# Kernel tuning notes

Measured on AMD Instinct MI355X. Metric: run time of the kernel, lower is better.

## Reference

```python
import jax, jax.numpy as jnp
import numpy as np

N_NODES = 50000
N_EDGES = 300000
D_IN = 256
D_OUT = 256


def setup_inputs() -> dict:
    key = jax.random.key(0)
    k1, k2, k3, k4 = jax.random.split(key, 4)
    x = jax.random.normal(k1, (N_NODES, D_IN), dtype=jnp.float32)
    edge_index = jax.random.randint(k2, (2, N_EDGES), 0, N_NODES, dtype=jnp.int64)
    edge_weight = jax.random.uniform(k3, (N_EDGES,), dtype=jnp.float32)
    # nn.Linear(D_IN, D_OUT, bias=False): weight shape [out, in]
    W = jax.random.normal(k4, (D_OUT, D_IN), dtype=jnp.float32) * (1.0 / np.sqrt(D_IN))
    return {"x": x, "edge_index": edge_index, "edge_weight": edge_weight, "W": W}


def reference(x, edge_index, edge_weight, W):
    # x = self.linear(x)  -> [N, D_OUT]
    x_proj = jnp.einsum("nd,od->no", x, W)
    # torch.sparse.mm(A_hat, x_proj): out[dst] += A[dst, src] * x_proj[src]
    dst = edge_index[0]
    src = edge_index[1]
    msgs = edge_weight[:, None] * x_proj[src]  # [E, D_OUT]
    out = jax.ops.segment_sum(msgs, dst, num_segments=N_NODES)
    return out
```

## Files before the change

kernel.cpp:

```cpp
#include <hip/hip_runtime.h>
#include <stdint.h>

#define D 256

typedef __bf16 bf16x8 __attribute__((ext_vector_type(8)));
typedef unsigned short u16x8 __attribute__((ext_vector_type(8)));
typedef float f32x4 __attribute__((ext_vector_type(4)));

static __device__ inline unsigned short f2bf(float f) {
    union { float f; unsigned u; } c; c.f = f;
    unsigned u = c.u + 0x7FFFu + ((c.u >> 16) & 1u);
    return (unsigned short)(u >> 16);
}
static __device__ inline float bf2f(unsigned short h) {
    union { unsigned u; float f; } c; c.u = (unsigned)h << 16;
    return c.f;
}

__global__ void count_kernel(const int* __restrict__ dst, int* __restrict__ cnt, int E) {
    int e = blockIdx.x * blockDim.x + threadIdx.x;
    if (e < E) atomicAdd(&cnt[dst[e]], 1);
}

__global__ __launch_bounds__(1024) void scan_local_kernel(const int* __restrict__ cnt,
        int* __restrict__ exsc, int* __restrict__ bsum, int n) {
    int t = threadIdx.x;
    int idx = blockIdx.x * 1024 + t;
    int v = (idx < n) ? cnt[idx] : 0;
    __shared__ int tmp[1024];
    tmp[t] = v;
    __syncthreads();
    for (int off = 1; off < 1024; off <<= 1) {
        int u = 0;
        if (t >= off) u = tmp[t - off];
        __syncthreads();
        tmp[t] += u;
        __syncthreads();
    }
    if (idx < n) exsc[idx] = tmp[t] - v;
    if (t == 1023) bsum[blockIdx.x] = tmp[t];
}

__global__ void scan_bsum_kernel(int* __restrict__ bsum, int nb) {
    int t = threadIdx.x;
    int orig = (t < nb) ? bsum[t] : 0;
    int v = orig;
    for (int off = 1; off < 64; off <<= 1) {
        int u = __shfl_up(v, off, 64);
        if (t >= off) v += u;
    }
    if (t < nb) bsum[t] = v - orig;
}

__global__ void scan_finalize_kernel(const int* __restrict__ exsc, const int* __restrict__ bsum,
        int* __restrict__ offs, int* __restrict__ cur, int n, int E) {
    int idx = blockIdx.x * blockDim.x + threadIdx.x;
    if (idx < n) {
        int o = exsc[idx] + bsum[idx >> 10];
        offs[idx] = o;
        cur[idx]  = o;
    }
    if (idx == 0) offs[n] = E;
}

__global__ void fill_kernel(const int* __restrict__ dst, const int* __restrict__ src,
        const float* __restrict__ ew, int* __restrict__ cur,
        int* __restrict__ srcS, float* __restrict__ wS, int E) {
    int e = blockIdx.x * blockDim.x + threadIdx.x;
    if (e < E) {
        int d = dst[e];
        int pos = atomicAdd(&cur[d], 1);
        srcS[pos] = src[e];
        wS[pos]   = ew[e];
    }
}

__global__ void wconv_kernel(const float* __restrict__ Wp, unsigned short* __restrict__ Wbf) {
    int f = blockIdx.x * 256 + threadIdx.x;
    if (f >= 8192) return;
    int n  = f >> 5;
    int k0 = (f & 31) << 3;
    const float4* p = (const float4*)(Wp + (size_t)n * D + k0);
    float4 v0 = p[0], v1 = p[1];
    u16x8 h;
    h[0] = f2bf(v0.x); h[1] = f2bf(v0.y); h[2] = f2bf(v0.z); h[3] = f2bf(v0.w);
    h[4] = f2bf(v1.x); h[5] = f2bf(v1.y); h[6] = f2bf(v1.z); h[7] = f2bf(v1.w);
    int t = n >> 4, l16 = n & 15;
    int s = k0 >> 5, q = (k0 >> 3) & 3;
    ((u16x8*)Wbf)[(t * 8 + s) * 64 + q * 16 + l16] = h;
}

__global__ __launch_bounds__(256, 2) void gemm2_kernel(
        const float* __restrict__ X, const unsigned short* __restrict__ Wbf,
        unsigned short* __restrict__ xproj, int M,
        const int* __restrict__ dst, const int* __restrict__ src,
        const float* __restrict__ ew, int* __restrict__ cur,
        int* __restrict__ srcS, float* __restrict__ wS, int E) {
    __shared__ u16x8 Asm[32 * 64];

    int tid = threadIdx.x;

    int stride = (int)gridDim.x * 256;
    for (int e = (int)blockIdx.x * 256 + tid; e < E; e += stride) {
        int d = dst[e];
        int pos = atomicAdd(&cur[d], 1);
        srcS[pos] = src[e];
        wS[pos]   = ew[e];
    }

    int m0  = (int)blockIdx.x * 64;
    int row = tid >> 2, akc = tid & 3;
    int grow = m0 + row; if (grow > M - 1) grow = M - 1;
    const float* ab = X + (size_t)grow * D + akc * 8;

#pragma unroll
    for (int s = 0; s < 8; ++s) {
        const float4* p = (const float4*)(ab + s * 32);
        float4 v0 = p[0], v1 = p[1];
        u16x8 h;
        h[0] = f2bf(v0.x); h[1] = f2bf(v0.y); h[2] = f2bf(v0.z); h[3] = f2bf(v0.w);
        h[4] = f2bf(v1.x); h[5] = f2bf(v1.y); h[6] = f2bf(v1.z); h[7] = f2bf(v1.w);
        Asm[(s * 4 + akc) * 64 + row] = h;
    }
    __syncthreads();

    int lane = tid & 63, wn = tid >> 6;
    int l16 = lane & 15, lq = lane >> 4;

    f32x4 acc[4][4];
#pragma unroll
    for (int i = 0; i < 4; ++i)
#pragma unroll
        for (int j = 0; j < 4; ++j)
            acc[i][j] = (f32x4){0.f, 0.f, 0.f, 0.f};

    const u16x8* wb = (const u16x8*)Wbf;
#pragma unroll
    for (int s = 0; s < 8; ++s) {
        u16x8 bfr[4], af[4];
#pragma unroll
        for (int fn = 0; fn < 4; ++fn)
            bfr[fn] = wb[((wn * 4 + fn) * 8 + s) * 64 + lane];
#pragma unroll
        for (int fm = 0; fm < 4; ++fm)
            af[fm] = Asm[(s * 4 + lq) * 64 + fm * 16 + l16];
#pragma unroll
        for (int fm = 0; fm < 4; ++fm)
#pragma unroll
            for (int fn = 0; fn < 4; ++fn)
                acc[fm][fn] = __builtin_amdgcn_mfma_f32_16x16x32_bf16(
                    __builtin_bit_cast(bf16x8, af[fm]),
                    __builtin_bit_cast(bf16x8, bfr[fn]),
                    acc[fm][fn], 0, 0, 0);
    }

    __syncthreads();
    unsigned short* Ls = (unsigned short*)Asm;
#pragma unroll
    for (int fm = 0; fm < 4; ++fm) {
        int r0 = fm * 16 + lq * 4;
#pragma unroll
        for (int fn = 0; fn < 4; ++fn) {
            int col = wn * 64 + fn * 16 + l16;
#pragma unroll
            for (int r = 0; r < 4; ++r)
                Ls[(r0 + r) * 256 + col] = f2bf(acc[fm][fn][r]);
        }
    }
    __syncthreads();
    const u16x8* Lv = (const u16x8*)Asm;
#pragma unroll
    for (int it = 0; it < 8; ++it) {
        int slot = it * 256 + tid;
        int r = slot >> 5, c8 = slot & 31;
        int orow = m0 + r;
        if (orow < M)
            ((u16x8*)(xproj + (size_t)orow * D))[c8] = Lv[slot];
    }
}

__global__ __launch_bounds__(256) void aggp_kernel(const ushort4* __restrict__ P,
        const int* __restrict__ offs, const int* __restrict__ srcS,
        const float* __restrict__ wS, float4* __restrict__ out4, int N) {
    int wave = threadIdx.x >> 6;
    int lane = threadIdx.x & 63;
    int node = blockIdx.x * 4 + wave;
    if (node >= N) return;
    int beg = offs[node], end = offs[node + 1];
    float ax = 0.f, ay = 0.f, az = 0.f, aw = 0.f;
    int e = beg;
    for (; e + 3 < end; e += 4) {
        int s0 = srcS[e], s1 = srcS[e + 1], s2 = srcS[e + 2], s3 = srcS[e + 3];
        float w0 = wS[e], w1 = wS[e + 1], w2 = wS[e + 2], w3 = wS[e + 3];
        ushort4 h0 = P[(size_t)s0 * 64 + lane];
        ushort4 h1 = P[(size_t)s1 * 64 + lane];
        ushort4 h2 = P[(size_t)s2 * 64 + lane];
        ushort4 h3 = P[(size_t)s3 * 64 + lane];
        ax += w0 * bf2f(h0.x); ay += w0 * bf2f(h0.y); az += w0 * bf2f(h0.z); aw += w0 * bf2f(h0.w);
        ax += w1 * bf2f(h1.x); ay += w1 * bf2f(h1.y); az += w1 * bf2f(h1.z); aw += w1 * bf2f(h1.w);
        ax += w2 * bf2f(h2.x); ay += w2 * bf2f(h2.y); az += w2 * bf2f(h2.z); aw += w2 * bf2f(h2.w);
        ax += w3 * bf2f(h3.x); ay += w3 * bf2f(h3.y); az += w3 * bf2f(h3.z); aw += w3 * bf2f(h3.w);
    }
    for (; e < end; ++e) {
        int s0 = srcS[e];
        float w0 = wS[e];
        ushort4 h0 = P[(size_t)s0 * 64 + lane];
        ax += w0 * bf2f(h0.x); ay += w0 * bf2f(h0.y); az += w0 * bf2f(h0.z); aw += w0 * bf2f(h0.w);
    }
    float4 r; r.x = ax; r.y = ay; r.z = az; r.w = aw;
    out4[(size_t)node * 64 + lane] = r;
}

__global__ __launch_bounds__(256) void agg_kernel(const float4* __restrict__ X4,
        const int* __restrict__ offs, const int* __restrict__ srcS,
        const float* __restrict__ wS, float4* __restrict__ agg4, int N) {
    int wave = threadIdx.x >> 6;
    int lane = threadIdx.x & 63;
    int node = blockIdx.x * 4 + wave;
    if (node >= N) return;
    int beg = offs[node], end = offs[node + 1];
    float ax = 0.f, ay = 0.f, az = 0.f, aw = 0.f;
    for (int e = beg; e < end; ++e) {
        int sN = srcS[e];
        float wt = wS[e];
        float4 xv = X4[(size_t)sN * 64 + lane];
        ax += wt * xv.x; ay += wt * xv.y; az += wt * xv.z; aw += wt * xv.w;
    }
    float4 r; r.x = ax; r.y = ay; r.z = az; r.w = aw;
    agg4[(size_t)node * 64 + lane] = r;
}

__global__ __launch_bounds__(256) void gemm_kernel(const float* __restrict__ A,
        const float* __restrict__ Wp, float* __restrict__ out, int M) {
    __shared__ u16x8 Asm[4 * 64];
    __shared__ u16x8 Bsm[4 * 256];
    int tid  = threadIdx.x;
    int lane = tid & 63;
    int wn   = tid >> 6;
    int m0   = blockIdx.x * 64;
    f32x4 acc[4][4];
#pragma unroll
    for (int i = 0; i < 4; ++i)
#pragma unroll
        for (int j = 0; j < 4; ++j)
            acc[i][j] = (f32x4){0.f, 0.f, 0.f, 0.f};
    int arow = tid >> 2;
    int akc  = tid & 3;
    int grow = m0 + arow; if (grow > M - 1) grow = M - 1;
    const float* aBase = A + (size_t)grow * D + akc * 8;
    int l16 = lane & 15, lq = lane >> 4;
    for (int s = 0; s < 8; ++s) {
        int k0 = s * 32;
        {
            const float4* p = (const float4*)(aBase + k0);
            float4 v0 = p[0], v1 = p[1];
            u16x8 h;
            h[0] = f2bf(v0.x); h[1] = f2bf(v0.y); h[2] = f2bf(v0.z); h[3] = f2bf(v0.w);
            h[4] = f2bf(v1.x); h[5] = f2bf(v1.y); h[6] = f2bf(v1.z); h[7] = f2bf(v1.w);
            Asm[akc * 64 + arow] = h;
        }
#pragma unroll
        for (int j = 0; j < 4; ++j) {
            int n = j * 64 + (tid >> 2);
            const float4* p = (const float4*)(Wp + (size_t)n * D + k0 + akc * 8);
            float4 v0 = p[0], v1 = p[1];
            u16x8 h;
            h[0] = f2bf(v0.x); h[1] = f2bf(v0.y); h[2] = f2bf(v0.z); h[3] = f2bf(v0.w);
            h[4] = f2bf(v1.x); h[5] = f2bf(v1.y); h[6] = f2bf(v1.z); h[7] = f2bf(v1.w);
            Bsm[akc * 256 + n] = h;
        }
        __syncthreads();
        u16x8 af[4], bfr[4];
#pragma unroll
        for (int fm = 0; fm < 4; ++fm) af[fm] = Asm[lq * 64 + fm * 16 + l16];
#pragma unroll
        for (int fn = 0; fn < 4; ++fn) bfr[fn] = Bsm[lq * 256 + wn * 64 + fn * 16 + l16];
#pragma unroll
        for (int fm = 0; fm < 4; ++fm)
#pragma unroll
            for (int fn = 0; fn < 4; ++fn)
                acc[fm][fn] = __builtin_amdgcn_mfma_f32_16x16x32_bf16(
                    __builtin_bit_cast(bf16x8, af[fm]),
                    __builtin_bit_cast(bf16x8, bfr[fn]),
                    acc[fm][fn], 0, 0, 0);
        __syncthreads();
    }
#pragma unroll
    for (int fm = 0; fm < 4; ++fm)
#pragma unroll
        for (int fn = 0; fn < 4; ++fn)
#pragma unroll
            for (int r = 0; r < 4; ++r) {
                int row = m0 + fm * 16 + lq * 4 + r;
                int col = wn * 64 + fn * 16 + l16;
                if (row < M) out[(size_t)row * D + col] = acc[fm][fn][r];
            }
}

extern "C" void kernel_launch(void* const* d_in, const int* in_sizes, int n_in,
                              void* d_out, int out_size, void* d_ws, size_t ws_size,
                              hipStream_t stream) {
    const float* X  = (const float*)d_in[0];
    const int*   ei = (const int*)d_in[1];
    const float* ew = (const float*)d_in[2];
    const float* Wp = (const float*)d_in[3];
    float* out = (float*)d_out;

    int N = in_sizes[0] / D;
    int E = in_sizes[2];
    const int* dst = ei;
    const int* src = ei + E;
    int nb = (N + 1023) / 1024;

    size_t xpBytes  = (size_t)N * D * sizeof(unsigned short);
    size_t wbBytes  = (size_t)D * D * sizeof(unsigned short);
    size_t csrInts  = (size_t)4 * N + 1 + nb + 2 * (size_t)E;
    size_t csrBytes = csrInts * sizeof(int);
    bool planB = (ws_size >= xpBytes + wbBytes + csrBytes + 512);

    uint8_t* ws = (uint8_t*)d_ws;
    unsigned short* xproj = (unsigned short*)ws;
    unsigned short* Wbf = (unsigned short*)(ws + ((xpBytes + 255) & ~(size_t)255));
    int* csr = planB ? (int*)((uint8_t*)Wbf + ((wbBytes + 255) & ~(size_t)255)) : (int*)ws;

    int* cnt  = csr;
    int* offs = cnt + N;
    int* cur  = offs + N + 1;
    int* srcS = cur + N;
    float* wS = (float*)(srcS + E);
    int* exsc = (int*)(wS + E);
    int* bsum = exsc + N;

    hipMemsetAsync(cnt, 0, (size_t)N * sizeof(int), stream);
    count_kernel<<<dim3((E + 255) / 256), dim3(256), 0, stream>>>(dst, cnt, E);
    scan_local_kernel<<<dim3(nb), dim3(1024), 0, stream>>>(cnt, exsc, bsum, N);
    scan_bsum_kernel<<<dim3(1), dim3(64), 0, stream>>>(bsum, nb);
    scan_finalize_kernel<<<dim3((N + 255) / 256), dim3(256), 0, stream>>>(exsc, bsum, offs, cur, N, E);

    if (planB) {
        wconv_kernel<<<dim3(32), dim3(256), 0, stream>>>(Wp, Wbf);
        gemm2_kernel<<<dim3((N + 63) / 64), dim3(256), 0, stream>>>(
            X, Wbf, xproj, N, dst, src, ew, cur, srcS, wS, E);
        aggp_kernel<<<dim3((N + 3) / 4), dim3(256), 0, stream>>>(
            (const ushort4*)xproj, offs, srcS, wS, (float4*)out, N);
    } else {
        fill_kernel<<<dim3((E + 255) / 256), dim3(256), 0, stream>>>(dst, src, ew, cur, srcS, wS, E);
        agg_kernel<<<dim3((N + 3) / 4), dim3(256), 0, stream>>>((const float4*)X, offs, srcS, wS,
                                                                (float4*)out, N);
        gemm_kernel<<<dim3((N + 63) / 64), dim3(256), 0, stream>>>(out, Wp, out, N);
    }
}
```

Before: 181.7 us.

## Fuse finalize with W conversion, split fill into separate blocks, pack CSR pairs

Merges the scan-finalize and weight bf16 conversion into one launch. In the GEMM, the grid-strided edge fill becomes dedicated extra blocks, B fragments are double-buffered from global, and the output staging is XOR-swizzled to reduce LDS bank conflicts. The CSR source index and weight are packed into one uint2 array so aggregation does a single 8-byte load per edge, and aggregation moves to 512-thread blocks. Each change removes a launch or memory latency but adds more blocks and changes occupancy.

```diff
diff --git a/kernel.cpp b/kernel.cpp
--- a/kernel.cpp
+++ b/kernel.cpp
@@ -52,6 +52,170 @@
     if (t < nb) bsum[t] = v - orig;
 }
 
+__global__ void finalize_wconv_kernel(const int* __restrict__ exsc, const int* __restrict__ bsum,
+        int* __restrict__ offs, int* __restrict__ cur, int n, int E, int finBlocks,
+        const float* __restrict__ Wp, unsigned short* __restrict__ Wbf) {
+    if ((int)blockIdx.x >= finBlocks) {
+        int f = ((int)blockIdx.x - finBlocks) * 256 + threadIdx.x;
+        if (f < 8192) {
+            int nr = f >> 5;
+            int k0 = (f & 31) << 3;
+            const float4* p = (const float4*)(Wp + (size_t)nr * D + k0);
+            float4 v0 = p[0], v1 = p[1];
+            u16x8 h;
+            h[0] = f2bf(v0.x); h[1] = f2bf(v0.y); h[2] = f2bf(v0.z); h[3] = f2bf(v0.w);
+            h[4] = f2bf(v1.x); h[5] = f2bf(v1.y); h[6] = f2bf(v1.z); h[7] = f2bf(v1.w);
+            int t = nr >> 4, l16 = nr & 15;
+            int s = k0 >> 5, q = (k0 >> 3) & 3;
+            ((u16x8*)Wbf)[(t * 8 + s) * 64 + q * 16 + l16] = h;
+        }
+        return;
+    }
+    int idx = (int)blockIdx.x * 256 + threadIdx.x;
+    if (idx < n) {
+        int o = exsc[idx] + bsum[idx >> 10];
+        offs[idx] = o;
+        cur[idx]  = o;
+    }
+    if (idx == 0) offs[n] = E;
+}
+
+__global__ __launch_bounds__(256, 3) void gemm3_kernel(
+        const float* __restrict__ X, const unsigned short* __restrict__ Wbf,
+        unsigned short* __restrict__ xproj, int M, int gemmBlocks,
+        const int* __restrict__ dst, const int* __restrict__ src,
+        const float* __restrict__ ew, int* __restrict__ cur,
+        uint2* __restrict__ pairS, int E) {
+    __shared__ u16x8 Asm[32 * 64];
+
+    int tid = threadIdx.x;
+
+    if ((int)blockIdx.x >= gemmBlocks) {
+        int e = ((int)blockIdx.x - gemmBlocks) * 256 + tid;
+        if (e < E) {
+            int d = dst[e];
+            int pos = atomicAdd(&cur[d], 1);
+            uint2 pk;
+            pk.x = (unsigned)src[e];
+            pk.y = __float_as_uint(ew[e]);
+            pairS[pos] = pk;
+        }
+        return;
+    }
+
+    int m0  = (int)blockIdx.x * 64;
+    int row = tid >> 2, akc = tid & 3;
+    int grow = m0 + row; if (grow > M - 1) grow = M - 1;
+    const float* ab = X + (size_t)grow * D + akc * 8;
+
+#pragma unroll
+    for (int s = 0; s < 8; ++s) {
+        const float4* p = (const float4*)(ab + s * 32);
+        float4 v0 = p[0], v1 = p[1];
+        u16x8 h;
+        h[0] = f2bf(v0.x); h[1] = f2bf(v0.y); h[2] = f2bf(v0.z); h[3] = f2bf(v0.w);
+        h[4] = f2bf(v1.x); h[5] = f2bf(v1.y); h[6] = f2bf(v1.z); h[7] = f2bf(v1.w);
+        Asm[(s * 4 + akc) * 64 + row] = h;
+    }
+    __syncthreads();
+
+    int lane = tid & 63, wn = tid >> 6;
+    int l16 = lane & 15, lq = lane >> 4;
+
+    f32x4 acc[4][4];
+#pragma unroll
+    for (int i = 0; i < 4; ++i)
+#pragma unroll
+        for (int j = 0; j < 4; ++j)
+            acc[i][j] = (f32x4){0.f, 0.f, 0.f, 0.f};
+
+    const u16x8* wbp = (const u16x8*)Wbf + (size_t)(wn * 32) * 64 + lane;
+    u16x8 bcur[4];
+#pragma unroll
+    for (int fn = 0; fn < 4; ++fn) bcur[fn] = wbp[(fn * 8) * 64];
+
+#pragma unroll
+    for (int s = 0; s < 8; ++s) {
+        u16x8 bnx[4];
+#pragma unroll
+        for (int fn = 0; fn < 4; ++fn)
+            bnx[fn] = wbp[(fn * 8 + ((s + 1) & 7)) * 64];
+        u16x8 af[4];
+#pragma unroll
+        for (int fm = 0; fm < 4; ++fm)
+            af[fm] = Asm[(s * 4 + lq) * 64 + fm * 16 + l16];
+#pragma unroll
+        for (int fm = 0; fm < 4; ++fm)
+#pragma unroll
+            for (int fn = 0; fn < 4; ++fn)
+                acc[fm][fn] = __builtin_amdgcn_mfma_f32_16x16x32_bf16(
+                    __builtin_bit_cast(bf16x8, af[fm]),
+                    __builtin_bit_cast(bf16x8, bcur[fn]),
+                    acc[fm][fn], 0, 0, 0);
+#pragma unroll
+        for (int fn = 0; fn < 4; ++fn) bcur[fn] = bnx[fn];
+    }
+
+    __syncthreads();
+    unsigned short* Ls = (unsigned short*)Asm;
+#pragma unroll
+    for (int fm = 0; fm < 4; ++fm) {
+        int r0 = fm * 16 + lq * 4;
+#pragma unroll
+        for (int fn = 0; fn < 4; ++fn) {
+            int cs = (wn * 64 + fn * 16 + l16) ^ (lq << 4);
+#pragma unroll
+            for (int r = 0; r < 4; ++r)
+                Ls[(r0 + r) * 256 + cs] = f2bf(acc[fm][fn][r]);
+        }
+    }
+    __syncthreads();
+    const u16x8* Lv = (const u16x8*)Asm;
+#pragma unroll
+    for (int it = 0; it < 8; ++it) {
+        int slot = it * 256 + tid;
+        int rr = slot >> 5, c8 = slot & 31;
+        int idx = rr * 32 + (c8 ^ (((rr >> 2) & 3) << 1));
+        int orow = m0 + rr;
+        if (orow < M)
+            ((u16x8*)(xproj + (size_t)orow * D))[c8] = Lv[idx];
+    }
+}
+
+__global__ __launch_bounds__(512) void aggp_kernel(const ushort4* __restrict__ P,
+        const int* __restrict__ offs, const uint2* __restrict__ pairS,
+        float4* __restrict__ out4, int N) {
+    int wave = threadIdx.x >> 6;
+    int lane = threadIdx.x & 63;
+    int node = blockIdx.x * 8 + wave;
+    if (node >= N) return;
+    int beg = offs[node], end = offs[node + 1];
+    float ax = 0.f, ay = 0.f, az = 0.f, aw = 0.f;
+    int e = beg;
+    for (; e + 3 < end; e += 4) {
+        uint2 p0 = pairS[e],     p1 = pairS[e + 1];
+        uint2 p2 = pairS[e + 2], p3 = pairS[e + 3];
+        float w0 = __uint_as_float(p0.y), w1 = __uint_as_float(p1.y);
+        float w2 = __uint_as_float(p2.y), w3 = __uint_as_float(p3.y);
+        ushort4 h0 = P[(size_t)p0.x * 64 + lane];
+        ushort4 h1 = P[(size_t)p1.x * 64 + lane];
+        ushort4 h2 = P[(size_t)p2.x * 64 + lane];
+        ushort4 h3 = P[(size_t)p3.x * 64 + lane];
+        ax += w0 * bf2f(h0.x); ay += w0 * bf2f(h0.y); az += w0 * bf2f(h0.z); aw += w0 * bf2f(h0.w);
+        ax += w1 * bf2f(h1.x); ay += w1 * bf2f(h1.y); az += w1 * bf2f(h1.z); aw += w1 * bf2f(h1.w);
+        ax += w2 * bf2f(h2.x); ay += w2 * bf2f(h2.y); az += w2 * bf2f(h2.z); aw += w2 * bf2f(h2.w);
+        ax += w3 * bf2f(h3.x); ay += w3 * bf2f(h3.y); az += w3 * bf2f(h3.z); aw += w3 * bf2f(h3.w);
+    }
+    for (; e < end; ++e) {
+        uint2 p0 = pairS[e];
+        float w0 = __uint_as_float(p0.y);
+        ushort4 h0 = P[(size_t)p0.x * 64 + lane];
+        ax += w0 * bf2f(h0.x); ay += w0 * bf2f(h0.y); az += w0 * bf2f(h0.z); aw += w0 * bf2f(h0.w);
+    }
+    float4 r; r.x = ax; r.y = ay; r.z = az; r.w = aw;
+    out4[(size_t)node * 64 + lane] = r;
+}
+
 __global__ void scan_finalize_kernel(const int* __restrict__ exsc, const int* __restrict__ bsum,
         int* __restrict__ offs, int* __restrict__ cur, int n, int E) {
     int idx = blockIdx.x * blockDim.x + threadIdx.x;
@@ -73,142 +237,6 @@
         srcS[pos] = src[e];
         wS[pos]   = ew[e];
     }
-}
-
-__global__ void wconv_kernel(const float* __restrict__ Wp, unsigned short* __restrict__ Wbf) {
-    int f = blockIdx.x * 256 + threadIdx.x;
-    if (f >= 8192) return;
-    int n  = f >> 5;
-    int k0 = (f & 31) << 3;
-    const float4* p = (const float4*)(Wp + (size_t)n * D + k0);
-    float4 v0 = p[0], v1 = p[1];
-    u16x8 h;
-    h[0] = f2bf(v0.x); h[1] = f2bf(v0.y); h[2] = f2bf(v0.z); h[3] = f2bf(v0.w);
-    h[4] = f2bf(v1.x); h[5] = f2bf(v1.y); h[6] = f2bf(v1.z); h[7] = f2bf(v1.w);
-    int t = n >> 4, l16 = n & 15;
-    int s = k0 >> 5, q = (k0 >> 3) & 3;
-    ((u16x8*)Wbf)[(t * 8 + s) * 64 + q * 16 + l16] = h;
-}
-
-__global__ __launch_bounds__(256, 2) void gemm2_kernel(
-        const float* __restrict__ X, const unsigned short* __restrict__ Wbf,
-        unsigned short* __restrict__ xproj, int M,
-        const int* __restrict__ dst, const int* __restrict__ src,
-        const float* __restrict__ ew, int* __restrict__ cur,
-        int* __restrict__ srcS, float* __restrict__ wS, int E) {
-    __shared__ u16x8 Asm[32 * 64];
-
-    int tid = threadIdx.x;
-
-    int stride = (int)gridDim.x * 256;
-    for (int e = (int)blockIdx.x * 256 + tid; e < E; e += stride) {
-        int d = dst[e];
-        int pos = atomicAdd(&cur[d], 1);
-        srcS[pos] = src[e];
-        wS[pos]   = ew[e];
-    }
-
-    int m0  = (int)blockIdx.x * 64;
-    int row = tid >> 2, akc = tid & 3;
-    int grow = m0 + row; if (grow > M - 1) grow = M - 1;
-    const float* ab = X + (size_t)grow * D + akc * 8;
-
-#pragma unroll
-    for (int s = 0; s < 8; ++s) {
-        const float4* p = (const float4*)(ab + s * 32);
-        float4 v0 = p[0], v1 = p[1];
-        u16x8 h;
-        h[0] = f2bf(v0.x); h[1] = f2bf(v0.y); h[2] = f2bf(v0.z); h[3] = f2bf(v0.w);
-        h[4] = f2bf(v1.x); h[5] = f2bf(v1.y); h[6] = f2bf(v1.z); h[7] = f2bf(v1.w);
-        Asm[(s * 4 + akc) * 64 + row] = h;
-    }
-    __syncthreads();
-
-    int lane = tid & 63, wn = tid >> 6;
-    int l16 = lane & 15, lq = lane >> 4;
-
-    f32x4 acc[4][4];
-#pragma unroll
-    for (int i = 0; i < 4; ++i)
-#pragma unroll
-        for (int j = 0; j < 4; ++j)
-            acc[i][j] = (f32x4){0.f, 0.f, 0.f, 0.f};
-
-    const u16x8* wb = (const u16x8*)Wbf;
-#pragma unroll
-    for (int s = 0; s < 8; ++s) {
-        u16x8 bfr[4], af[4];
-#pragma unroll
-        for (int fn = 0; fn < 4; ++fn)
-            bfr[fn] = wb[((wn * 4 + fn) * 8 + s) * 64 + lane];
-#pragma unroll
-        for (int fm = 0; fm < 4; ++fm)
-            af[fm] = Asm[(s * 4 + lq) * 64 + fm * 16 + l16];
-#pragma unroll
-        for (int fm = 0; fm < 4; ++fm)
-#pragma unroll
-            for (int fn = 0; fn < 4; ++fn)
-                acc[fm][fn] = __builtin_amdgcn_mfma_f32_16x16x32_bf16(
-                    __builtin_bit_cast(bf16x8, af[fm]),
-                    __builtin_bit_cast(bf16x8, bfr[fn]),
-                    acc[fm][fn], 0, 0, 0);
-    }
-
-    __syncthreads();
-    unsigned short* Ls = (unsigned short*)Asm;
-#pragma unroll
-    for (int fm = 0; fm < 4; ++fm) {
-        int r0 = fm * 16 + lq * 4;
-#pragma unroll
-        for (int fn = 0; fn < 4; ++fn) {
-            int col = wn * 64 + fn * 16 + l16;
-#pragma unroll
-            for (int r = 0; r < 4; ++r)
-                Ls[(r0 + r) * 256 + col] = f2bf(acc[fm][fn][r]);
-        }
-    }
-    __syncthreads();
-    const u16x8* Lv = (const u16x8*)Asm;
-#pragma unroll
-    for (int it = 0; it < 8; ++it) {
-        int slot = it * 256 + tid;
-        int r = slot >> 5, c8 = slot & 31;
-        int orow = m0 + r;
-        if (orow < M)
-            ((u16x8*)(xproj + (size_t)orow * D))[c8] = Lv[slot];
-    }
-}
-
-__global__ __launch_bounds__(256) void aggp_kernel(const ushort4* __restrict__ P,
-        const int* __restrict__ offs, const int* __restrict__ srcS,
-        const float* __restrict__ wS, float4* __restrict__ out4, int N) {
-    int wave = threadIdx.x >> 6;
-    int lane = threadIdx.x & 63;
-    int node = blockIdx.x * 4 + wave;
-    if (node >= N) return;
-    int beg = offs[node], end = offs[node + 1];
-    float ax = 0.f, ay = 0.f, az = 0.f, aw = 0.f;
-    int e = beg;
-    for (; e + 3 < end; e += 4) {
-        int s0 = srcS[e], s1 = srcS[e + 1], s2 = srcS[e + 2], s3 = srcS[e + 3];
-        float w0 = wS[e], w1 = wS[e + 1], w2 = wS[e + 2], w3 = wS[e + 3];
-        ushort4 h0 = P[(size_t)s0 * 64 + lane];
-        ushort4 h1 = P[(size_t)s1 * 64 + lane];
-        ushort4 h2 = P[(size_t)s2 * 64 + lane];
-        ushort4 h3 = P[(size_t)s3 * 64 + lane];
-        ax += w0 * bf2f(h0.x); ay += w0 * bf2f(h0.y); az += w0 * bf2f(h0.z); aw += w0 * bf2f(h0.w);
-        ax += w1 * bf2f(h1.x); ay += w1 * bf2f(h1.y); az += w1 * bf2f(h1.z); aw += w1 * bf2f(h1.w);
-        ax += w2 * bf2f(h2.x); ay += w2 * bf2f(h2.y); az += w2 * bf2f(h2.z); aw += w2 * bf2f(h2.w);
-        ax += w3 * bf2f(h3.x); ay += w3 * bf2f(h3.y); az += w3 * bf2f(h3.z); aw += w3 * bf2f(h3.w);
-    }
-    for (; e < end; ++e) {
-        int s0 = srcS[e];
-        float w0 = wS[e];
-        ushort4 h0 = P[(size_t)s0 * 64 + lane];
-        ax += w0 * bf2f(h0.x); ay += w0 * bf2f(h0.y); az += w0 * bf2f(h0.z); aw += w0 * bf2f(h0.w);
-    }
-    float4 r; r.x = ax; r.y = ay; r.z = az; r.w = aw;
-    out4[(size_t)node * 64 + lane] = r;
 }
 
 __global__ __launch_bounds__(256) void agg_kernel(const float4* __restrict__ X4,
@@ -326,24 +354,30 @@
     int* cnt  = csr;
     int* offs = cnt + N;
     int* cur  = offs + N + 1;
-    int* srcS = cur + N;
+    int* edg  = cur + N;
+    uint2* pairS = (uint2*)edg;
+    int* srcS = edg;
     float* wS = (float*)(srcS + E);
-    int* exsc = (int*)(wS + E);
+    int* exsc = (int*)(edg + 2 * (size_t)E);
     int* bsum = exsc + N;
 
     hipMemsetAsync(cnt, 0, (size_t)N * sizeof(int), stream);
     count_kernel<<<dim3((E + 255) / 256), dim3(256), 0, stream>>>(dst, cnt, E);
     scan_local_kernel<<<dim3(nb), dim3(1024), 0, stream>>>(cnt, exsc, bsum, N);
     scan_bsum_kernel<<<dim3(1), dim3(64), 0, stream>>>(bsum, nb);
-    scan_finalize_kernel<<<dim3((N + 255) / 256), dim3(256), 0, stream>>>(exsc, bsum, offs, cur, N, E);
 
     if (planB) {
-        wconv_kernel<<<dim3(32), dim3(256), 0, stream>>>(Wp, Wbf);
-        gemm2_kernel<<<dim3((N + 63) / 64), dim3(256), 0, stream>>>(
-            X, Wbf, xproj, N, dst, src, ew, cur, srcS, wS, E);
-        aggp_kernel<<<dim3((N + 3) / 4), dim3(256), 0, stream>>>(
-            (const ushort4*)xproj, offs, srcS, wS, (float4*)out, N);
+        int finBlocks = (N + 255) / 256;
+        finalize_wconv_kernel<<<dim3(finBlocks + 32), dim3(256), 0, stream>>>(
+            exsc, bsum, offs, cur, N, E, finBlocks, Wp, Wbf);
+        int gemmBlocks = (N + 63) / 64;
+        int fillBlocks = (E + 255) / 256;
+        gemm3_kernel<<<dim3(gemmBlocks + fillBlocks), dim3(256), 0, stream>>>(
+            X, Wbf, xproj, N, gemmBlocks, dst, src, ew, cur, pairS, E);
+        aggp_kernel<<<dim3((N + 7) / 8), dim3(512), 0, stream>>>(
+            (const ushort4*)xproj, offs, pairS, (float4*)out, N);
     } else {
+        scan_finalize_kernel<<<dim3((N + 255) / 256), dim3(256), 0, stream>>>(exsc, bsum, offs, cur, N, E);
         fill_kernel<<<dim3((E + 255) / 256), dim3(256), 0, stream>>>(dst, src, ew, cur, srcS, wS, E);
         agg_kernel<<<dim3((N + 3) / 4), dim3(256), 0, stream>>>((const float4*)X, offs, srcS, wS,
                                                                 (float4*)out, N);
```

New measurement: 169.7 us. -6.6%, faster.
